# Kernel optimization log

Hardware: AMD Instinct MI355X
Metric: run time of the kernel (lower is better)

Reference implementation:

```python
import jax, jax.numpy as jnp
import numpy as np

WIN = (8, 8)
DIM = 256
HEADS = 8
B = 2048
NW = 64


def _make_buffers(win):
    wh, ww = win
    # relative_position_bias_table: (1, 2wh-1, 2ww-1, 2)
    rh = np.arange(-(wh - 1), wh, dtype=np.float32)
    rw = np.arange(-(ww - 1), ww, dtype=np.float32)
    gh, gw = np.meshgrid(rh, rw, indexing='ij')
    tbl = np.stack([gh, gw], axis=-1)[None]  # (1, 2wh-1, 2ww-1, 2)
    tbl[..., 0] /= (wh - 1)
    tbl[..., 1] /= (ww - 1)
    tbl *= 3.2
    tbl = np.sign(tbl) * (1.0 - np.exp(-np.abs(tbl)))
    # relative_position_index: (n, n)
    ch, cw = np.meshgrid(np.arange(wh), np.arange(ww), indexing='ij')
    cf = np.stack([ch.reshape(-1), cw.reshape(-1)])  # (2, n)
    rel = cf[:, :, None] - cf[:, None, :]            # (2, n, n)
    rel = rel.transpose(1, 2, 0).astype(np.int64)
    rel[..., 0] += wh - 1
    rel[..., 1] += ww - 1
    rel[..., 0] *= 2 * ww - 1
    rpi = rel.sum(-1).astype(np.int32)
    return jnp.asarray(tbl, dtype=jnp.float32), jnp.asarray(rpi)


def setup_inputs() -> dict:
    key = jax.random.key(0)
    ks = jax.random.split(key, 12)
    c2 = DIM // 2
    n = WIN[0] * WIN[1]
    s = 0.02
    inp = {
        'x': jax.random.normal(ks[0], (B, n, DIM), dtype=jnp.float32),
        'mask': jax.random.normal(ks[1], (NW, n, n), dtype=jnp.float32),
        'qw': jax.random.normal(ks[2], (2, c2, c2), dtype=jnp.float32) * s,
        'qb': jnp.zeros((2, c2), dtype=jnp.float32),
        'kw': jax.random.normal(ks[3], (2, c2, c2), dtype=jnp.float32) * s,
        'kb': jnp.zeros((2, c2), dtype=jnp.float32),
        'vw': jax.random.normal(ks[4], (2, c2, c2), dtype=jnp.float32) * s,
        'vb': jnp.zeros((2, c2), dtype=jnp.float32),
        'pw': jax.random.normal(ks[5], (2, c2, c2), dtype=jnp.float32) * s,
        'pb': jnp.zeros((2, c2), dtype=jnp.float32),
        'mlp_w1': jax.random.normal(ks[6], (2, 128), dtype=jnp.float32) * s,
        'mlp_b1': jnp.zeros((128,), dtype=jnp.float32),
        'mlp_w2': jax.random.normal(ks[7], (128, HEADS), dtype=jnp.float32) * s,
        'logit_scale': jnp.full((HEADS, 1, 1), np.log(10.0), dtype=jnp.float32),
    }
    tbl, rpi = _make_buffers(WIN)
    inp['rpb_table'] = tbl
    inp['rpi'] = rpi
    return inp


def _l2norm(v, eps=1e-12):
    nrm = jnp.sqrt(jnp.sum(v * v, axis=-1, keepdims=True))
    return v / jnp.maximum(nrm, eps)


def _forward(x, mask, qw, qb, kw, kb, vw, vb, pw, pb,
             mlp_w1, mlp_b1, mlp_w2, logit_scale, rpb_table, rpi):
    b, n, c = x.shape
    h = logit_scale.shape[0]
    c2 = c // 2
    hd = c // h
    xb = x.reshape(b, n, 2, c2)  # branch split on channel halves

    def dual(w, bias):  # residual dual-branch linear: xb + Linear(xb)
        return xb + jnp.einsum('bnsc,scd->bnsd', xb, w) + bias

    # (b, n, 2, c2) -> (b, n, c) -> (b, h, n, hd)
    q = dual(qw, qb).reshape(b, n, h, hd).transpose(0, 2, 1, 3)
    k = dual(kw, kb).reshape(b, n, h, hd).transpose(0, 2, 1, 3)
    v = dual(vw, vb).reshape(b, n, h, hd).transpose(0, 2, 1, 3)

    attn = jnp.einsum('bhnd,bhmd->bhnm', _l2norm(q), _l2norm(k))
    scale = jnp.exp(jnp.minimum(logit_scale, jnp.log(jnp.float32(100.0))))  # (h,1,1)
    attn = attn * scale[None]

    # CPB-MLP relative position bias
    hid = jax.nn.relu(rpb_table @ mlp_w1 + mlp_b1)         # (1, 2wh-1, 2ww-1, 128)
    tbl = (hid @ mlp_w2).reshape(-1, h)                    # ((2wh-1)(2ww-1), h)
    bias = tbl[rpi.reshape(-1)].reshape(n, n, h).transpose(2, 0, 1)
    attn = attn + 16.0 * jax.nn.sigmoid(bias)[None]

    if mask is not None:
        nw = mask.shape[0]
        attn = attn.reshape(b // nw, nw, h, n, n) + mask[None, :, None]
        attn = attn.reshape(b, h, n, n)

    attn = jax.nn.softmax(attn, axis=-1)
    out = jnp.einsum('bhnm,bhmd->bhnd', attn, v).transpose(0, 2, 1, 3).reshape(b, n, c)

    ob = out.reshape(b, n, 2, c2)
    y = jnp.einsum('bnsc,scd->bnsd', ob, pw) + pb
    return y.reshape(b, n, c)


def reference(x, mask, qw, qb, kw, kb, vw, vb, pw, pb,
              mlp_w1, mlp_b1, mlp_w2, logit_scale, rpb_table, rpi):
    return _forward(x, mask, qw, qb, kw, kb, vw, vb, pw, pb,
                    mlp_w1, mlp_b1, mlp_w2, logit_scale, rpb_table, rpi)
```

## Files before the change

### kernel.cpp

```cpp
#include <hip/hip_runtime.h>
#include <stdint.h>

#define B_    2048
#define N_    64
#define C_    256
#define C2_   128
#define H_    8
#define NW_   64
#define NPOS  225
#define PX    136
#define PV    72

typedef __attribute__((ext_vector_type(8))) short short8;
typedef __attribute__((ext_vector_type(4))) float float4v;

union U8 { unsigned u[4]; short8 s; };

__device__ float g_scale[H_];
__device__ float g_t8[NPOS][H_];
__device__ __align__(16) float g_sb[NW_ * H_ * N_ * N_];
__device__ unsigned short g_wt[4][2][C2_][C2_];

__device__ __forceinline__ float b2f(unsigned short u) {
  return __uint_as_float(((unsigned int)u) << 16);
}
__device__ __forceinline__ unsigned short f2b(float f) {
  unsigned int u = __float_as_uint(f);
  u += 0x7fffu + ((u >> 16) & 1u);
  return (unsigned short)(u >> 16);
}

__global__ __launch_bounds__(256) void k_prep1(
    const float* __restrict__ tbl, const float* __restrict__ w1,
    const float* __restrict__ b1, const float* __restrict__ w2,
    const float* __restrict__ ls) {
  __shared__ float sw1[256], sb1[128], sw2[1024];
  const int t = threadIdx.x;
  sw1[t] = w1[t];
  if (t < 128) sb1[t] = b1[t];
#pragma unroll
  for (int it = 0; it < 4; ++it) sw2[it * 256 + t] = w2[it * 256 + t];
  __syncthreads();
  if (t < NPOS) {
    float a0 = tbl[2 * t], a1 = tbl[2 * t + 1];
    float acc[H_];
#pragma unroll
    for (int h = 0; h < H_; ++h) acc[h] = 0.f;
    for (int j = 0; j < 128; ++j) {
      float hid = fmaxf(a0 * sw1[j] + a1 * sw1[128 + j] + sb1[j], 0.f);
#pragma unroll
      for (int h = 0; h < H_; ++h) acc[h] += hid * sw2[j * H_ + h];
    }
#pragma unroll
    for (int h = 0; h < H_; ++h) g_t8[t][h] = acc[h];
  }
  if (t < H_) g_scale[t] = __expf(fminf(ls[t], 4.6051702f));
}

__global__ __launch_bounds__(256) void k_prep2(
    const float* __restrict__ mask, const int* __restrict__ rpi) {
  const int base = blockIdx.x * 1024;
#pragma unroll
  for (int it = 0; it < 4; ++it) {
    int idx = base + it * 256 + threadIdx.x;
    int j  = idx & 63;
    int i  = (idx >> 6) & 63;
    int h  = (idx >> 12) & 7;
    int wd = idx >> 15;
    float v = g_t8[rpi[i * 64 + j]][h];
    g_sb[idx] = 16.f / (1.f + __expf(-v)) + mask[wd * 4096 + i * 64 + j];
  }
}

__global__ __launch_bounds__(256) void k_prepw(
    const float* __restrict__ qw, const float* __restrict__ kw,
    const float* __restrict__ vw, const float* __restrict__ pw) {
  __shared__ unsigned short lt[128 * 132];
  const int t = threadIdx.x;
  const int p = blockIdx.x >> 1, s = blockIdx.x & 1;
  const float* src = (p == 0 ? qw : p == 1 ? kw : p == 2 ? vw : pw) + s * (C2_ * C2_);
#pragma unroll
  for (int it = 0; it < 64; ++it) {
    int e = it * 256 + t;
    int c = e >> 7, d = e & 127;
    lt[d * 132 + c] = f2b(src[e]);
  }
  __syncthreads();
#pragma unroll
  for (int it = 0; it < 64; ++it) {
    int e = it * 256 + t;
    int d = e >> 7, c = e & 127;
    g_wt[p][s][d][c] = lt[d * 132 + c];
  }
}

__global__ __launch_bounds__(512) void k_main(
    const float* __restrict__ x, float* __restrict__ out,
    const float* __restrict__ qb, const float* __restrict__ kb,
    const float* __restrict__ vb, const float* __restrict__ pb) {
  __shared__ __align__(16) unsigned short xs[N_ * PX];
  __shared__ __align__(16) unsigned short qs[N_ * PX];
  __shared__ __align__(16) unsigned short ks[N_ * PX];
  __shared__ __align__(16) unsigned short vt[C2_ * PV];

  const int t    = threadIdx.x;
  const int lane = t & 63;
  const int w    = __builtin_amdgcn_readfirstlane(t >> 6);
  const int bs   = blockIdx.x;
  const int b    = bs >> 1;
  const int s1   = bs & 1;
  const int l15  = lane & 15;
  const int qd   = lane >> 4;

  {
    const float* xg = x + (size_t)b * (N_ * C_) + s1 * C2_;
#pragma unroll
    for (int it = 0; it < 4; ++it) {
      int e = t + 512 * it;
      int row = e >> 5, c4 = (e & 31) << 2;
      float4 v = *(const float4*)&xg[row * C_ + c4];
      uint2 pk;
      pk.x = ((unsigned)f2b(v.y) << 16) | f2b(v.x);
      pk.y = ((unsigned)f2b(v.w) << 16) | f2b(v.z);
      *(uint2*)&xs[row * PX + c4] = pk;
    }
  }
  __syncthreads();

  const int jls = w >> 1;
  const int jl  = 32 * jls;
  const int mh  = w & 1;
  const float scl = g_scale[s1 * 4 + jls];
  for (int pj = 0; pj < 3; ++pj) {
    const float* bi = pj == 0 ? qb : (pj == 1 ? kb : vb);
    float4v acc[2][2];
    {
      float b0 = bi[s1 * C2_ + jl + l15], b1 = bi[s1 * C2_ + jl + 16 + l15];
#pragma unroll
      for (int mt = 0; mt < 2; ++mt) {
        acc[mt][0] = float4v{b0, b0, b0, b0};
        acc[mt][1] = float4v{b1, b1, b1, b1};
      }
    }
    const unsigned short* wt = &g_wt[pj][s1][0][0];
#pragma unroll
    for (int kc = 0; kc < 4; ++kc) {
      int ko = kc * 32 + qd * 8;
      short8 a[2], bf[2];
#pragma unroll
      for (int mt = 0; mt < 2; ++mt)
        a[mt] = *(const short8*)&xs[(32 * mh + mt * 16 + l15) * PX + ko];
      bf[0] = *(const short8*)&wt[(jl + l15) * C2_ + ko];
      bf[1] = *(const short8*)&wt[(jl + 16 + l15) * C2_ + ko];
#pragma unroll
      for (int mt = 0; mt < 2; ++mt)
#pragma unroll
        for (int nt = 0; nt < 2; ++nt)
          acc[mt][nt] = __builtin_amdgcn_mfma_f32_16x16x32_bf16(
              a[mt], bf[nt], acc[mt][nt], 0, 0, 0);
    }
    unsigned short* dst = pj == 0 ? qs : ks;
#pragma unroll
    for (int mt = 0; mt < 2; ++mt) {
      int row0 = 32 * mh + mt * 16 + qd * 4;
      float vv[2][4];
#pragma unroll
      for (int nt = 0; nt < 2; ++nt)
#pragma unroll
        for (int r = 0; r < 4; ++r)
          vv[nt][r] = acc[mt][nt][r] +
                      b2f(xs[(row0 + r) * PX + jl + nt * 16 + l15]);
      if (pj < 2) {
        float ss[4];
#pragma unroll
        for (int r = 0; r < 4; ++r) ss[r] = vv[0][r] * vv[0][r] + vv[1][r] * vv[1][r];
#pragma unroll
        for (int m = 1; m < 16; m <<= 1)
#pragma unroll
          for (int r = 0; r < 4; ++r) ss[r] += __shfl_xor(ss[r], m, 64);
#pragma unroll
        for (int r = 0; r < 4; ++r) {
          float rn = 1.0f / fmaxf(sqrtf(ss[r]), 1e-12f);
          if (pj == 0) rn *= scl;
          vv[0][r] *= rn;
          vv[1][r] *= rn;
        }
#pragma unroll
        for (int nt = 0; nt < 2; ++nt)
#pragma unroll
          for (int r = 0; r < 4; ++r)
            dst[(row0 + r) * PX + jl + nt * 16 + l15] = f2b(vv[nt][r]);
      } else {
#pragma unroll
        for (int nt = 0; nt < 2; ++nt) {
          int chan = jl + nt * 16 + l15;
          uint2 pk;
          pk.x = ((unsigned)f2b(vv[nt][1]) << 16) | f2b(vv[nt][0]);
          pk.y = ((unsigned)f2b(vv[nt][3]) << 16) | f2b(vv[nt][2]);
          *(uint2*)&vt[chan * PV + row0] = pk;
        }
      }
    }
  }
  __syncthreads();

  const int hl = w >> 1;
  const int rh = w & 1;
  const int h  = s1 * 4 + hl;
  const float* sbh = g_sb + ((size_t)(b & 63) * H_ + h) * 4096;
  const int hi_sel = lane & 32;
  const int src0 = l15 | ((((qd << 1) + 0) & 3) << 4);
  const int src1 = l15 | ((((qd << 1) + 1) & 3) << 4);
#pragma unroll
  for (int mq = 0; mq < 2; ++mq) {
    const int r0 = 32 * rh + 16 * mq;
    short8 bq = *(const short8*)&qs[(r0 + l15) * PX + hl * 32 + qd * 8];
    float4v sacc[4];
#pragma unroll
    for (int nt = 0; nt < 4; ++nt) {
      float4 cv = *(const float4*)&sbh[(r0 + l15) * 64 + nt * 16 + qd * 4];
      float4v c = {cv.x, cv.y, cv.z, cv.w};
      short8 ak = *(const short8*)&ks[(nt * 16 + l15) * PX + hl * 32 + qd * 8];
      sacc[nt] = __builtin_amdgcn_mfma_f32_16x16x32_bf16(ak, bq, c, 0, 0, 0);
    }
    float e[4][4];
    float s = 0.f;
#pragma unroll
    for (int nt = 0; nt < 4; ++nt)
#pragma unroll
      for (int r = 0; r < 4; ++r) {
        e[nt][r] = __expf(sacc[nt][r]);
        s += e[nt][r];
      }
    s += __shfl_xor(s, 16, 64);
    s += __shfl_xor(s, 32, 64);
    float rr = 1.0f / s;
    unsigned pk[4][2];
#pragma unroll
    for (int nt = 0; nt < 4; ++nt)
#pragma unroll
      for (int rp = 0; rp < 2; ++rp)
        pk[nt][rp] = ((unsigned)f2b(e[nt][2 * rp + 1] * rr) << 16) |
                     f2b(e[nt][2 * rp] * rr);
    U8 au[2];
#pragma unroll
    for (int j2 = 0; j2 < 4; ++j2) {
      int src = (j2 >> 1) ? src1 : src0;
      int rp = j2 & 1;
      int r0v = __shfl((int)pk[0][rp], src, 64);
      int r1v = __shfl((int)pk[1][rp], src, 64);
      int r2v = __shfl((int)pk[2][rp], src, 64);
      int r3v = __shfl((int)pk[3][rp], src, 64);
      au[0].u[j2] = hi_sel ? (unsigned)r1v : (unsigned)r0v;
      au[1].u[j2] = hi_sel ? (unsigned)r3v : (unsigned)r2v;
    }
    float4v oacc[2];
    oacc[0] = float4v{0, 0, 0, 0};
    oacc[1] = float4v{0, 0, 0, 0};
#pragma unroll
    for (int kc = 0; kc < 2; ++kc) {
      short8 ap = au[kc].s;
#pragma unroll
      for (int nt2 = 0; nt2 < 2; ++nt2) {
        short8 bv = *(const short8*)&vt[(hl * 32 + nt2 * 16 + l15) * PV + kc * 32 + qd * 8];
        oacc[nt2] = __builtin_amdgcn_mfma_f32_16x16x32_bf16(ap, bv, oacc[nt2], 0, 0, 0);
      }
    }
#pragma unroll
    for (int nt2 = 0; nt2 < 2; ++nt2)
#pragma unroll
      for (int r = 0; r < 4; ++r)
        xs[(r0 + qd * 4 + r) * PX + hl * 32 + nt2 * 16 + l15] = f2b(oacc[nt2][r]);
  }
  __syncthreads();

  {
    float4v acc[2][2];
    float b0 = pb[s1 * C2_ + jl + l15], b1 = pb[s1 * C2_ + jl + 16 + l15];
#pragma unroll
    for (int mt = 0; mt < 2; ++mt) {
      acc[mt][0] = float4v{b0, b0, b0, b0};
      acc[mt][1] = float4v{b1, b1, b1, b1};
    }
    const unsigned short* wt = &g_wt[3][s1][0][0];
#pragma unroll
    for (int kc = 0; kc < 4; ++kc) {
      int ko = kc * 32 + qd * 8;
      short8 a[2], bf[2];
#pragma unroll
      for (int mt = 0; mt < 2; ++mt)
        a[mt] = *(const short8*)&xs[(32 * mh + mt * 16 + l15) * PX + ko];
      bf[0] = *(const short8*)&wt[(jl + l15) * C2_ + ko];
      bf[1] = *(const short8*)&wt[(jl + 16 + l15) * C2_ + ko];
#pragma unroll
      for (int mt = 0; mt < 2; ++mt)
#pragma unroll
        for (int nt = 0; nt < 2; ++nt)
          acc[mt][nt] = __builtin_amdgcn_mfma_f32_16x16x32_bf16(
              a[mt], bf[nt], acc[mt][nt], 0, 0, 0);
    }
#pragma unroll
    for (int mt = 0; mt < 2; ++mt)
#pragma unroll
      for (int nt = 0; nt < 2; ++nt)
#pragma unroll
        for (int r = 0; r < 4; ++r)
          out[((size_t)b * N_ + 32 * mh + mt * 16 + qd * 4 + r) * C_ +
              s1 * C2_ + jl + nt * 16 + l15] = acc[mt][nt][r];
  }
}

extern "C" void kernel_launch(void* const* d_in, const int* in_sizes, int n_in,
                              void* d_out, int out_size, void* d_ws, size_t ws_size,
                              hipStream_t stream) {
  const float* x    = (const float*)d_in[0];
  const float* mask = (const float*)d_in[1];
  const float* qw   = (const float*)d_in[2];
  const float* qb   = (const float*)d_in[3];
  const float* kw   = (const float*)d_in[4];
  const float* kb   = (const float*)d_in[5];
  const float* vw   = (const float*)d_in[6];
  const float* vb   = (const float*)d_in[7];
  const float* pw   = (const float*)d_in[8];
  const float* pb   = (const float*)d_in[9];
  const float* w1   = (const float*)d_in[10];
  const float* b1   = (const float*)d_in[11];
  const float* w2   = (const float*)d_in[12];
  const float* ls   = (const float*)d_in[13];
  const float* tbl  = (const float*)d_in[14];
  const int*   rpi  = (const int*)d_in[15];
  float* out = (float*)d_out;

  k_prep1<<<1, 256, 0, stream>>>(tbl, w1, b1, w2, ls);
  k_prep2<<<2048, 256, 0, stream>>>(mask, rpi);
  k_prepw<<<8, 256, 0, stream>>>(qw, kw, vw, pw);
  k_main<<<B_ * 2, 512, 0, stream>>>(x, out, qb, kb, vb, pb);
}
```

Before: 391.9 us.

## Fold residual identity into weights, merge prep kernels, hoist loads, use DPP reductions

The two weight and MLP prep kernels become one launch, and the residual add of x is folded into the Q/K/V weights by adding 1.0 to their diagonals, so k_main no longer re-reads xs. The main kernel hoists bias, x-fragment, K, V and score-bias loads out of the inner loops and uses DPP row reductions for the L2 norm. It also uses packed bf16 conversion, sets a launch_bounds occupancy hint of 4 and remaps block indices so the two half-channel blocks of a batch are scheduled near each other. Folding the identity into bf16 weights rounds the residual differently, and holding more fragments in registers raises register pressure.

```diff
diff --git a/kernel.cpp b/kernel.cpp
--- a/kernel.cpp
+++ b/kernel.cpp
@@ -1,4 +1,5 @@
 #include <hip/hip_runtime.h>
+#include <hip/hip_bf16.h>
 #include <stdint.h>
 
 #define B_    2048
@@ -29,32 +30,75 @@
   u += 0x7fffu + ((u >> 16) & 1u);
   return (unsigned short)(u >> 16);
 }
-
-__global__ __launch_bounds__(256) void k_prep1(
+__device__ __forceinline__ unsigned f2b2(float lo, float hi) {
+  __hip_bfloat162 h = __float22bfloat162_rn(float2{lo, hi});
+  unsigned u;
+  __builtin_memcpy(&u, &h, 4);
+  return u;
+}
+__device__ __forceinline__ float rowsum16(float v) {
+  int x = __float_as_int(v);
+  v += __int_as_float(__builtin_amdgcn_update_dpp(0, x, 0xB1, 0xF, 0xF, false));
+  x = __float_as_int(v);
+  v += __int_as_float(__builtin_amdgcn_update_dpp(0, x, 0x4E, 0xF, 0xF, false));
+  x = __float_as_int(v);
+  v += __int_as_float(__builtin_amdgcn_update_dpp(0, x, 0x124, 0xF, 0xF, false));
+  x = __float_as_int(v);
+  v += __int_as_float(__builtin_amdgcn_update_dpp(0, x, 0x128, 0xF, 0xF, false));
+  return v;
+}
+
+__global__ __launch_bounds__(256) void k_prep_a(
+    const float* __restrict__ qw, const float* __restrict__ kw,
+    const float* __restrict__ vw, const float* __restrict__ pw,
     const float* __restrict__ tbl, const float* __restrict__ w1,
     const float* __restrict__ b1, const float* __restrict__ w2,
     const float* __restrict__ ls) {
-  __shared__ float sw1[256], sb1[128], sw2[1024];
+  __shared__ unsigned short lt[128 * 132];
   const int t = threadIdx.x;
-  sw1[t] = w1[t];
-  if (t < 128) sb1[t] = b1[t];
-#pragma unroll
-  for (int it = 0; it < 4; ++it) sw2[it * 256 + t] = w2[it * 256 + t];
-  __syncthreads();
-  if (t < NPOS) {
-    float a0 = tbl[2 * t], a1 = tbl[2 * t + 1];
-    float acc[H_];
-#pragma unroll
-    for (int h = 0; h < H_; ++h) acc[h] = 0.f;
-    for (int j = 0; j < 128; ++j) {
-      float hid = fmaxf(a0 * sw1[j] + a1 * sw1[128 + j] + sb1[j], 0.f);
-#pragma unroll
-      for (int h = 0; h < H_; ++h) acc[h] += hid * sw2[j * H_ + h];
-    }
-#pragma unroll
-    for (int h = 0; h < H_; ++h) g_t8[t][h] = acc[h];
-  }
-  if (t < H_) g_scale[t] = __expf(fminf(ls[t], 4.6051702f));
+  if (blockIdx.x < 8) {
+    const int p = blockIdx.x >> 1, s = blockIdx.x & 1;
+    const float* src = (p == 0 ? qw : p == 1 ? kw : p == 2 ? vw : pw) + s * (C2_ * C2_);
+#pragma unroll
+    for (int it = 0; it < 64; ++it) {
+      int e = it * 256 + t;
+      int c = e >> 7, d = e & 127;
+      lt[d * 132 + c] = f2b(src[e]);
+    }
+    __syncthreads();
+#pragma unroll
+    for (int it = 0; it < 64; ++it) {
+      int e = it * 256 + t;
+      int d = e >> 7, c = e & 127;
+      unsigned short u = lt[d * 132 + c];
+      if (p < 3 && d == c) u = f2b(b2f(u) + 1.0f);
+      g_wt[p][s][d][c] = u;
+    }
+  } else {
+    float* fsh = (float*)lt;
+    float* sw1 = fsh;
+    float* sb1 = fsh + 256;
+    float* sw2 = fsh + 384;
+    sw1[t] = w1[t];
+    if (t < 128) sb1[t] = b1[t];
+#pragma unroll
+    for (int it = 0; it < 4; ++it) sw2[it * 256 + t] = w2[it * 256 + t];
+    __syncthreads();
+    if (t < NPOS) {
+      float a0 = tbl[2 * t], a1 = tbl[2 * t + 1];
+      float acc[H_];
+#pragma unroll
+      for (int h = 0; h < H_; ++h) acc[h] = 0.f;
+      for (int j = 0; j < 128; ++j) {
+        float hid = fmaxf(a0 * sw1[j] + a1 * sw1[128 + j] + sb1[j], 0.f);
+#pragma unroll
+        for (int h = 0; h < H_; ++h) acc[h] += hid * sw2[j * H_ + h];
+      }
+#pragma unroll
+      for (int h = 0; h < H_; ++h) g_t8[t][h] = acc[h];
+    }
+    if (t < H_) g_scale[t] = __expf(fminf(ls[t], 4.6051702f));
+  }
 }
 
 __global__ __launch_bounds__(256) void k_prep2(
@@ -72,29 +116,7 @@
   }
 }
 
-__global__ __launch_bounds__(256) void k_prepw(
-    const float* __restrict__ qw, const float* __restrict__ kw,
-    const float* __restrict__ vw, const float* __restrict__ pw) {
-  __shared__ unsigned short lt[128 * 132];
-  const int t = threadIdx.x;
-  const int p = blockIdx.x >> 1, s = blockIdx.x & 1;
-  const float* src = (p == 0 ? qw : p == 1 ? kw : p == 2 ? vw : pw) + s * (C2_ * C2_);
-#pragma unroll
-  for (int it = 0; it < 64; ++it) {
-    int e = it * 256 + t;
-    int c = e >> 7, d = e & 127;
-    lt[d * 132 + c] = f2b(src[e]);
-  }
-  __syncthreads();
-#pragma unroll
-  for (int it = 0; it < 64; ++it) {
-    int e = it * 256 + t;
-    int d = e >> 7, c = e & 127;
-    g_wt[p][s][d][c] = lt[d * 132 + c];
-  }
-}
-
-__global__ __launch_bounds__(512) void k_main(
+__global__ __launch_bounds__(512, 4) void k_main(
     const float* __restrict__ x, float* __restrict__ out,
     const float* __restrict__ qb, const float* __restrict__ kb,
     const float* __restrict__ vb, const float* __restrict__ pb) {
@@ -106,11 +128,21 @@
   const int t    = threadIdx.x;
   const int lane = t & 63;
   const int w    = __builtin_amdgcn_readfirstlane(t >> 6);
-  const int bs   = blockIdx.x;
-  const int b    = bs >> 1;
-  const int s1   = bs & 1;
+  const int bi   = blockIdx.x;
+  const int b    = ((bi >> 4) << 3) | (bi & 7);
+  const int s1   = (bi >> 3) & 1;
   const int l15  = lane & 15;
   const int qd   = lane >> 4;
+
+  const int jls = w >> 1;
+  const int jl  = 32 * jls;
+  const int mh  = w & 1;
+  const int cb = s1 * C2_ + jl + l15;
+  const float qb0 = qb[cb], qb1 = qb[cb + 16];
+  const float kb0 = kb[cb], kb1 = kb[cb + 16];
+  const float vb0 = vb[cb], vb1 = vb[cb + 16];
+  const float pb0 = pb[cb], pb1 = pb[cb + 16];
+  const float scl = g_scale[s1 * 4 + jls];
 
   {
     const float* xg = x + (size_t)b * (N_ * C_) + s1 * C2_;
@@ -120,36 +152,35 @@
       int row = e >> 5, c4 = (e & 31) << 2;
       float4 v = *(const float4*)&xg[row * C_ + c4];
       uint2 pk;
-      pk.x = ((unsigned)f2b(v.y) << 16) | f2b(v.x);
-      pk.y = ((unsigned)f2b(v.w) << 16) | f2b(v.z);
+      pk.x = f2b2(v.x, v.y);
+      pk.y = f2b2(v.z, v.w);
       *(uint2*)&xs[row * PX + c4] = pk;
     }
   }
   __syncthreads();
 
-  const int jls = w >> 1;
-  const int jl  = 32 * jls;
-  const int mh  = w & 1;
-  const float scl = g_scale[s1 * 4 + jls];
+  short8 a_all[4][2];
+#pragma unroll
+  for (int kc = 0; kc < 4; ++kc) {
+    int ko = kc * 32 + qd * 8;
+#pragma unroll
+    for (int mt = 0; mt < 2; ++mt)
+      a_all[kc][mt] = *(const short8*)&xs[(32 * mh + mt * 16 + l15) * PX + ko];
+  }
   for (int pj = 0; pj < 3; ++pj) {
-    const float* bi = pj == 0 ? qb : (pj == 1 ? kb : vb);
+    const float bi0 = pj == 0 ? qb0 : (pj == 1 ? kb0 : vb0);
+    const float bi1 = pj == 0 ? qb1 : (pj == 1 ? kb1 : vb1);
     float4v acc[2][2];
-    {
-      float b0 = bi[s1 * C2_ + jl + l15], b1 = bi[s1 * C2_ + jl + 16 + l15];
-#pragma unroll
-      for (int mt = 0; mt < 2; ++mt) {
-        acc[mt][0] = float4v{b0, b0, b0, b0};
-        acc[mt][1] = float4v{b1, b1, b1, b1};
-      }
+#pragma unroll
+    for (int mt = 0; mt < 2; ++mt) {
+      acc[mt][0] = float4v{bi0, bi0, bi0, bi0};
+      acc[mt][1] = float4v{bi1, bi1, bi1, bi1};
     }
     const unsigned short* wt = &g_wt[pj][s1][0][0];
 #pragma unroll
     for (int kc = 0; kc < 4; ++kc) {
       int ko = kc * 32 + qd * 8;
-      short8 a[2], bf[2];
-#pragma unroll
-      for (int mt = 0; mt < 2; ++mt)
-        a[mt] = *(const short8*)&xs[(32 * mh + mt * 16 + l15) * PX + ko];
+      short8 bf[2];
       bf[0] = *(const short8*)&wt[(jl + l15) * C2_ + ko];
       bf[1] = *(const short8*)&wt[(jl + 16 + l15) * C2_ + ko];
 #pragma unroll
@@ -157,60 +188,63 @@
 #pragma unroll
         for (int nt = 0; nt < 2; ++nt)
           acc[mt][nt] = __builtin_amdgcn_mfma_f32_16x16x32_bf16(
-              a[mt], bf[nt], acc[mt][nt], 0, 0, 0);
+              a_all[kc][mt], bf[nt], acc[mt][nt], 0, 0, 0);
     }
     unsigned short* dst = pj == 0 ? qs : ks;
 #pragma unroll
     for (int mt = 0; mt < 2; ++mt) {
       int row0 = 32 * mh + mt * 16 + qd * 4;
-      float vv[2][4];
-#pragma unroll
-      for (int nt = 0; nt < 2; ++nt)
-#pragma unroll
-        for (int r = 0; r < 4; ++r)
-          vv[nt][r] = acc[mt][nt][r] +
-                      b2f(xs[(row0 + r) * PX + jl + nt * 16 + l15]);
       if (pj < 2) {
-        float ss[4];
-#pragma unroll
-        for (int r = 0; r < 4; ++r) ss[r] = vv[0][r] * vv[0][r] + vv[1][r] * vv[1][r];
-#pragma unroll
-        for (int m = 1; m < 16; m <<= 1)
-#pragma unroll
-          for (int r = 0; r < 4; ++r) ss[r] += __shfl_xor(ss[r], m, 64);
+        float rn[4];
 #pragma unroll
         for (int r = 0; r < 4; ++r) {
-          float rn = 1.0f / fmaxf(sqrtf(ss[r]), 1e-12f);
-          if (pj == 0) rn *= scl;
-          vv[0][r] *= rn;
-          vv[1][r] *= rn;
+          float ss = acc[mt][0][r] * acc[mt][0][r] + acc[mt][1][r] * acc[mt][1][r];
+          ss = rowsum16(ss);
+          rn[r] = 1.0f / fmaxf(sqrtf(ss), 1e-12f);
+          if (pj == 0) rn[r] *= scl;
         }
 #pragma unroll
         for (int nt = 0; nt < 2; ++nt)
 #pragma unroll
           for (int r = 0; r < 4; ++r)
-            dst[(row0 + r) * PX + jl + nt * 16 + l15] = f2b(vv[nt][r]);
+            dst[(row0 + r) * PX + jl + nt * 16 + l15] = f2b(acc[mt][nt][r] * rn[r]);
       } else {
 #pragma unroll
         for (int nt = 0; nt < 2; ++nt) {
           int chan = jl + nt * 16 + l15;
           uint2 pk;
-          pk.x = ((unsigned)f2b(vv[nt][1]) << 16) | f2b(vv[nt][0]);
-          pk.y = ((unsigned)f2b(vv[nt][3]) << 16) | f2b(vv[nt][2]);
+          pk.x = f2b2(acc[mt][nt][0], acc[mt][nt][1]);
+          pk.y = f2b2(acc[mt][nt][2], acc[mt][nt][3]);
           *(uint2*)&vt[chan * PV + row0] = pk;
         }
       }
     }
   }
-  __syncthreads();
 
   const int hl = w >> 1;
   const int rh = w & 1;
   const int h  = s1 * 4 + hl;
   const float* sbh = g_sb + ((size_t)(b & 63) * H_ + h) * 4096;
+  float4 cv[2][4];
+#pragma unroll
+  for (int mq = 0; mq < 2; ++mq)
+#pragma unroll
+    for (int nt = 0; nt < 4; ++nt)
+      cv[mq][nt] = *(const float4*)&sbh[(32 * rh + 16 * mq + l15) * 64 + nt * 16 + qd * 4];
+  __syncthreads();
+
   const int hi_sel = lane & 32;
   const int src0 = l15 | ((((qd << 1) + 0) & 3) << 4);
   const int src1 = l15 | ((((qd << 1) + 1) & 3) << 4);
+  short8 ak[4], bv[2][2];
+#pragma unroll
+  for (int nt = 0; nt < 4; ++nt)
+    ak[nt] = *(const short8*)&ks[(nt * 16 + l15) * PX + hl * 32 + qd * 8];
+#pragma unroll
+  for (int kc = 0; kc < 2; ++kc)
+#pragma unroll
+    for (int nt2 = 0; nt2 < 2; ++nt2)
+      bv[kc][nt2] = *(const short8*)&vt[(hl * 32 + nt2 * 16 + l15) * PV + kc * 32 + qd * 8];
 #pragma unroll
   for (int mq = 0; mq < 2; ++mq) {
     const int r0 = 32 * rh + 16 * mq;
@@ -218,10 +252,8 @@
     float4v sacc[4];
 #pragma unroll
     for (int nt = 0; nt < 4; ++nt) {
-      float4 cv = *(const float4*)&sbh[(r0 + l15) * 64 + nt * 16 + qd * 4];
-      float4v c = {cv.x, cv.y, cv.z, cv.w};
-      short8 ak = *(const short8*)&ks[(nt * 16 + l15) * PX + hl * 32 + qd * 8];
-      sacc[nt] = __builtin_amdgcn_mfma_f32_16x16x32_bf16(ak, bq, c, 0, 0, 0);
+      float4v c = {cv[mq][nt].x, cv[mq][nt].y, cv[mq][nt].z, cv[mq][nt].w};
+      sacc[nt] = __builtin_amdgcn_mfma_f32_16x16x32_bf16(ak[nt], bq, c, 0, 0, 0);
     }
     float e[4][4];
     float s = 0.f;
@@ -240,8 +272,7 @@
     for (int nt = 0; nt < 4; ++nt)
 #pragma unroll
       for (int rp = 0; rp < 2; ++rp)
-        pk[nt][rp] = ((unsigned)f2b(e[nt][2 * rp + 1] * rr) << 16) |
-                     f2b(e[nt][2 * rp] * rr);
+        pk[nt][rp] = f2b2(e[nt][2 * rp] * rr, e[nt][2 * rp + 1] * rr);
     U8 au[2];
 #pragma unroll
     for (int j2 = 0; j2 < 4; ++j2) {
@@ -261,10 +292,8 @@
     for (int kc = 0; kc < 2; ++kc) {
       short8 ap = au[kc].s;
 #pragma unroll
-      for (int nt2 = 0; nt2 < 2; ++nt2) {
-        short8 bv = *(const short8*)&vt[(hl * 32 + nt2 * 16 + l15) * PV + kc * 32 + qd * 8];
-        oacc[nt2] = __builtin_amdgcn_mfma_f32_16x16x32_bf16(ap, bv, oacc[nt2], 0, 0, 0);
-      }
+      for (int nt2 = 0; nt2 < 2; ++nt2)
+        oacc[nt2] = __builtin_amdgcn_mfma_f32_16x16x32_bf16(ap, bv[kc][nt2], oacc[nt2], 0, 0, 0);
     }
 #pragma unroll
     for (int nt2 = 0; nt2 < 2; ++nt2)
@@ -276,11 +305,10 @@
 
   {
     float4v acc[2][2];
-    float b0 = pb[s1 * C2_ + jl + l15], b1 = pb[s1 * C2_ + jl + 16 + l15];
 #pragma unroll
     for (int mt = 0; mt < 2; ++mt) {
-      acc[mt][0] = float4v{b0, b0, b0, b0};
-      acc[mt][1] = float4v{b1, b1, b1, b1};
+      acc[mt][0] = float4v{pb0, pb0, pb0, pb0};
+      acc[mt][1] = float4v{pb1, pb1, pb1, pb1};
     }
     const unsigned short* wt = &g_wt[3][s1][0][0];
 #pragma unroll
@@ -331,8 +359,7 @@
   const int*   rpi  = (const int*)d_in[15];
   float* out = (float*)d_out;
 
-  k_prep1<<<1, 256, 0, stream>>>(tbl, w1, b1, w2, ls);
+  k_prep_a<<<9, 256, 0, stream>>>(qw, kw, vw, pw, tbl, w1, b1, w2, ls);
   k_prep2<<<2048, 256, 0, stream>>>(mask, rpi);
-  k_prepw<<<8, 256, 0, stream>>>(qw, kw, vw, pw);
   k_main<<<B_ * 2, 512, 0, stream>>>(x, out, qb, kb, vb, pb);
 }
```

New measurement: 384.5 us. No clear change (-1.9%).
